# Performance work log

Measured on AMD Instinct MI355X. Metric: run time of the kernel, lower is better.

The kernel has to match this reference:

```python
import jax, jax.numpy as jnp
import numpy as np

MAX_DF = 0.05
MAX_DPHI = 0.5
MAX_DA = 0.5
MIN_LENGTH = 2
N_BASE = 9
NEG = -jnp.inf


def _wrap(x):
    return (x + jnp.pi) % (2 * jnp.pi) - jnp.pi


def _link_single(tok):
    """tok: (W, K, 9) -> (new_tok9 (W,K,9), member (W,K) int32 local chain id or -1, count int32)."""
    W, K, _ = tok.shape
    snr = tok[..., 0]
    f_s, f_e = tok[..., 3], tok[..., 4]
    A_s, A_e = tok[..., 5], tok[..., 6]
    ps, pe = tok[..., 7], tok[..., 8]

    # ---- edge compatibility mask E[w, kp, kn] for w in 0..W-2 ----
    fe = f_e[:-1, :, None]; fs = f_s[1:, None, :]
    fm = (fe + fs) * 0.5
    f_ok = ~((fm > 0) & (jnp.abs(fe - fs) / jnp.where(fm > 0, fm, 1.0) > MAX_DF))
    p_ok = jnp.abs(_wrap(ps[1:, None, :] - pe[:-1, :, None])) <= MAX_DPHI
    ae = A_e[:-1, :, None]; an = A_s[1:, None, :]
    am = jnp.maximum(ae, an)
    a_ok = ~((am > 0) & (jnp.abs(ae - an) / jnp.where(am > 0, am, 1.0) > MAX_DA))
    E = (snr[:-1, :, None] > 0) & (snr[1:, None, :] > 0) & f_ok & p_ok & a_ok

    # ---- DP over windows: best-SNR chain ending at (w,k), seeded ONLY at window 0
    # (the torch code adds singletons for w>=1 AFTER the DP, so they never extend) ----
    best0 = jnp.where(snr[0] > 0, snr[0], NEG)

    def dp_step(best_prev, inp):
        Ew, snr_next = inp
        cand = jnp.where(Ew, best_prev[:, None] + snr_next[None, :], NEG)
        best_edge = cand.max(axis=0)
        arg = cand.argmax(axis=0).astype(jnp.int32)  # first max == smallest kp (torch tie rule)
        has = best_edge > NEG
        best_new = jnp.where(has, best_edge, NEG)
        return best_new, (best_new, jnp.where(has, arg, -1))

    _, (best_rest, pred_rest) = jax.lax.scan(dp_step, best0, (E, snr[1:]))
    best_dp = jnp.concatenate([best0[None], best_rest], 0)        # (W,K)
    pred = jnp.concatenate([jnp.full((1, K), -1, jnp.int32), pred_rest], 0)

    reach = best_dp > NEG
    # positive-snr tokens unreachable from window 0 become length-1 singleton chains
    score = jnp.where(reach, best_dp, jnp.where(snr > 0, snr, NEG))
    valid = score > NEG

    # ---- chain lengths ----
    def len_step(Lprev, inp):
        pw, vw = inp
        L = jnp.where(pw >= 0, Lprev[jnp.clip(pw, 0, K - 1)] + 1,
                      jnp.where(vw, 1, 0))
        return L, L

    L0 = jnp.where(valid[0], 1, 0).astype(jnp.int32)
    _, Lr = jax.lax.scan(len_step, L0, (pred[1:], valid[1:]))
    L = jnp.concatenate([L0[None], Lr], 0)                        # (W,K) int32

    # ---- backtrack token path for every endpoint: bpath[e, s] = token at window w_e - s ----
    def backtrack(w, k):
        def step(carry, _):
            cw, ck = carry
            nk = jnp.where((ck >= 0) & (cw > 0),
                           pred[jnp.clip(cw, 0, W - 1), jnp.clip(ck, 0, K - 1)], -1)
            return (cw - 1, nk), ck
        _, bp = jax.lax.scan(step, (w, k), None, length=W)
        return bp

    Wg, Kg = jnp.meshgrid(jnp.arange(W, dtype=jnp.int32),
                          jnp.arange(K, dtype=jnp.int32), indexing='ij')
    bpath = jax.vmap(backtrack)(Wg.reshape(-1), Kg.reshape(-1))   # (W*K, W) int32

    # ---- greedy non-overlapping assignment by descending total SNR ----
    order = jnp.argsort(-score.reshape(-1))  # stable; -inf endpoints sort last
    s_arr = jnp.arange(W)
    flatL = L.reshape(-1)
    flatV = valid.reshape(-1)

    def greedy_step(carry, e):
        used, counter = carry
        we = e // K
        Le = flatL[e]
        bp = bpath[e]
        act = s_arr < Le
        rows = jnp.where(act, we - s_arr, W)          # OOB rows dropped
        cols = jnp.clip(bp, 0, K - 1)
        M = jnp.zeros((W, K), bool).at[rows, cols].set(act, mode='drop')
        take = flatV[e] & ~jnp.any(M & used)
        used = used | (M & take)
        enrich = take & (Le >= MIN_LENGTH)
        cid = jnp.where(enrich, counter, -1)
        counter = counter + enrich.astype(jnp.int32)
        return (used, counter), (enrich, cid)

    (_, count), (enrich_o, cid_o) = jax.lax.scan(
        greedy_step, (jnp.zeros((W, K), bool), jnp.int32(0)), order)
    enrich = jnp.zeros((W * K,), bool).at[order].set(enrich_o)
    cid = jnp.full((W * K,), -1, jnp.int32).at[order].set(cid_o)

    # ---- per-slot membership + within-chain successor token (slots are disjoint) ----
    act = enrich[:, None] & (s_arr[None, :] < flatL[:, None])     # (W*K, W)
    we_all = (jnp.arange(W * K, dtype=jnp.int32) // K)[:, None]
    rows = jnp.where(act, we_all - s_arr[None, :], W)
    cols = jnp.clip(bpath, 0, K - 1)
    member = jnp.full((W, K), -1, jnp.int32).at[rows, cols].set(
        jnp.broadcast_to(cid[:, None], act.shape), mode='drop')
    succ_vals = jnp.concatenate(
        [jnp.full((W * K, 1), -1, jnp.int32), bpath[:, :-1].astype(jnp.int32)], 1)
    succ = jnp.full((W, K), -1, jnp.int32).at[rows, cols].set(succ_vals, mode='drop')

    # ---- enrichment 1: combined SNR = sqrt(sum snr^2) over each chain ----
    is_mem = member >= 0
    seg = jnp.where(is_mem, member, W * K)            # dummy segment for non-members
    snr2 = jnp.where(is_mem, snr * snr, 0.0)
    chain_snr2 = jax.ops.segment_sum(snr2.reshape(-1), seg.reshape(-1),
                                     num_segments=W * K + 1)
    safe = jnp.where(chain_snr2 > 0, chain_snr2, 1.0)
    snr_new = jnp.where(is_mem, jnp.sqrt(safe)[seg], snr)

    # ---- enrichment 2: boundary smoothing. Each boundary touches disjoint fields,
    # so all boundaries of all chains are independent and fully vectorizable. ----
    has_succ = succ >= 0
    nk = jnp.clip(succ, 0, K - 1)

    def nxt(col):  # value of col at (w+1, succ[w,k])
        shifted = jnp.concatenate([col[1:], jnp.zeros((1, K), col.dtype)], 0)
        return jnp.take_along_axis(shifted, nk, axis=1)

    f_avg = (f_e + nxt(f_s)) * 0.5
    A_avg = (A_e + nxt(A_s)) * 0.5
    ps_n = nxt(ps)
    corr = _wrap(ps_n - pe)
    f_e_new = jnp.where(has_succ, f_avg, f_e)
    A_e_new = jnp.where(has_succ, A_avg, A_e)
    pe_new = jnp.where(has_succ, pe + corr * 0.5, pe)
    rows2 = jnp.where(has_succ, jnp.arange(W)[:, None] + 1, W)
    f_s_new = f_s.at[rows2, nk].set(jnp.where(has_succ, f_avg, 0.0), mode='drop')
    A_s_new = A_s.at[rows2, nk].set(jnp.where(has_succ, A_avg, 0.0), mode='drop')
    ps_new = ps.at[rows2, nk].set(jnp.where(has_succ, ps_n - corr * 0.5, 0.0), mode='drop')

    out9 = jnp.stack([snr_new, tok[..., 1], tok[..., 2], f_s_new, f_e_new,
                      A_s_new, A_e_new, ps_new, pe_new], axis=-1)
    return out9, member, count


def setup_inputs() -> dict:
    key = jax.random.key(0)
    B, W, K, C = 16, 128, 32, 9
    tokens = jax.random.normal(key, (B, W, K, C), dtype=jnp.float32)
    return {"tokens": tokens}


def reference(tokens):
    new9, member, counts = jax.vmap(_link_single)(tokens[..., :N_BASE])
    # chain_counter carries across batch elements
    offsets = jnp.concatenate(
        [jnp.zeros((1,), counts.dtype), jnp.cumsum(counts)[:-1]])
    cid = jnp.where(member >= 0, member + offsets[:, None, None], -1)
    return jnp.concatenate([new9, cid[..., None].astype(tokens.dtype)], -1)
```

## Files before the change

### kernel.cpp

```cpp
#include <hip/hip_runtime.h>
#include <stdint.h>

#define WW 128
#define KK 32
#define NC 9
#define NCELL (WW * KK)
#define SLICES 16
#define BURN_TICKS 1200

__device__ __forceinline__ float wrapf(float x) {
  const float kPi = 3.14159265358979323846f;
  const float kTwoPi = 6.28318530717958647692f;
  float y = fmodf(x + kPi, kTwoPi);
  y = (y < 0.0f) ? (y + kTwoPi) : y;
  return y - kPi;
}

__device__ __forceinline__ uint32_t ordf(float f) {
  uint32_t u = __float_as_uint(f);
  return (u & 0x80000000u) ? ~u : (u | 0x80000000u);
}

__device__ __forceinline__ uint32_t hs_key(int j) {
  return 0x5EED0C0Du ^ ((uint32_t)j * 0x9E3779B9u);
}

struct Row {
  float snr, fs, fe, As, Ae, ps, pe;
};

__device__ __forceinline__ Row loadRow(const float* __restrict__ T, int w,
                                       int k) {
  const float* C = T + (size_t)(w * KK + k) * NC;
  Row r;
  r.snr = C[0];
  r.fs = C[3];
  r.fe = C[4];
  r.As = C[5];
  r.Ae = C[6];
  r.ps = C[7];
  r.pe = C[8];
  return r;
}

__global__ __launch_bounds__(256) void fused_kernel(
    const float* __restrict__ tokens, float* __restrict__ out,
    uint32_t* __restrict__ ws_u) {
  const uint64_t t_entry = __builtin_amdgcn_s_memrealtime();
  const int bb = blockIdx.x >> 4;
  const int sl = blockIdx.x & (SLICES - 1);
  const int tid = threadIdx.x;
  uint32_t* flags = ws_u;
  uint32_t* flags2 = ws_u + 64;
  uint32_t* chsum = ws_u + 256;
  int* packed = (int*)(ws_u + 4096);
  const float* T = tokens + (size_t)bb * NCELL * NC;

  __shared__ int8_t s_pred[NCELL];
  __shared__ int8_t s_member[NCELL];
  __shared__ int8_t s_succ[NCELL];
  __shared__ int8_t s_predcol[NCELL];
  __shared__ int8_t s_chaincol[KK * WW];
  __shared__ int s_chainlen[KK];
  __shared__ float s_chainsum[KK];
  __shared__ unsigned long long s_win[KK];
  __shared__ int s_count;
  __shared__ int s_wlim;
  __shared__ int s_cnt[64];
  __shared__ int s_mywl;

  const int i = (sl << 8) + tid;
  const int wcell = i >> 5;
  float t0, t1, t2, t3, t4, t5, t6, t7, t8;
  if (sl != 0) {
    const float* C = T + (size_t)i * NC;
    t0 = C[0]; t1 = C[1]; t2 = C[2]; t3 = C[3]; t4 = C[4];
    t5 = C[5]; t6 = C[6]; t7 = C[7]; t8 = C[8];
  }

  if (sl == 0) {
    {
      int* mi = (int*)s_member;
      int* si = (int*)s_succ;
      int* pi = (int*)s_predcol;
      for (int j = tid; j < NCELL / 4; j += 256) {
        mi[j] = -1;
        si[j] = -1;
        pi[j] = -1;
      }
      if (tid < KK) s_win[tid] = 0ull;
    }
    __syncthreads();

    if (tid < 64) {
      const int k = tid & 31;
      const int h = tid >> 5;
      float snr0 = T[k * NC + 0];
      bool v0 = snr0 > 0.0f;
      float prev_best = v0 ? snr0 : -INFINITY;
      int prev_root = k;
      float prev_fe = T[k * NC + 4];
      float prev_Ae = T[k * NC + 6];
      float prev_pe = T[k * NC + 8];
      if (h == 0) {
        s_pred[k] = -1;
        if (v0) {
          unsigned long long key =
              ((unsigned long long)ordf(snr0) << 32) | (uint32_t)(~(uint32_t)k);
          atomicMax(&s_win[k], key);
        }
      }
      Row cur = loadRow(T, 1, k);
      Row nxt = loadRow(T, 2, k);
      for (int w = 1; w < WW; ++w) {
        unsigned long long full = __ballot(prev_best > -INFINITY);
        if (full == 0ull) break;

        int wf = (w + 2 < WW) ? (w + 2) : (WW - 1);
        Row fut = loadRow(T, wf, k);

        bool scur = cur.snr > 0.0f;
        float bestE = -INFINITY;
        int arg = 0;
        unsigned int rem = (unsigned int)full;
        while (rem) {
          int kp0 = __ffs(rem) - 1;
          rem &= rem - 1;
          bool have2 = rem != 0u;
          int kp1 = have2 ? (__ffs(rem) - 1) : kp0;
          if (have2) rem &= rem - 1;
          int kp = h ? kp1 : kp0;
          bool lane_ok = h ? have2 : true;
          float bp = __shfl(prev_best, kp);
          float fe = __shfl(prev_fe, kp);
          float ae = __shfl(prev_Ae, kp);
          float pe = __shfl(prev_pe, kp);
          float fm = (fe + cur.fs) * 0.5f;
          float fden = (fm > 0.0f) ? fm : 1.0f;
          bool fbad = (fm > 0.0f) && (fabsf(fe - cur.fs) / fden > 0.05f);
          float am = fmaxf(ae, cur.As);
          float aden = (am > 0.0f) ? am : 1.0f;
          bool abad = (am > 0.0f) && (fabsf(ae - cur.As) / aden > 0.5f);
          bool pok = fabsf(wrapf(cur.ps - pe)) <= 0.5f;
          if (lane_ok && scur && !fbad && !abad && pok) {
            float cand = bp + cur.snr;
            if (cand > bestE) { bestE = cand; arg = kp; }
          }
        }
        float ob = __shfl_xor(bestE, 32);
        int oa = __shfl_xor(arg, 32);
        float b0 = h ? ob : bestE;
        float b1 = h ? bestE : ob;
        int a0 = h ? oa : arg;
        int a1 = h ? arg : oa;
        bool take0 = (b0 > b1) || ((b0 == b1) && (a0 <= a1));
        float bE = take0 ? b0 : b1;
        int aC = take0 ? a0 : a1;
        bool has = bE > -INFINITY;
        if (h == 0) s_pred[w * KK + k] = (int8_t)(has ? aC : -1);
        int rootc = __shfl(prev_root, has ? aC : 0);
        int root_new = has ? rootc : k;
        if (has && h == 0) {
          int idx = w * KK + k;
          unsigned long long key = ((unsigned long long)ordf(bE) << 32) |
                                   (uint32_t)(~(uint32_t)idx);
          atomicMax(&s_win[root_new], key);
        }
        prev_best = has ? bE : -INFINITY;
        prev_root = root_new;
        prev_fe = cur.fe;
        prev_Ae = cur.Ae;
        prev_pe = cur.pe;
        cur = nxt;
        nxt = fut;
      }
    }
    __syncthreads();

    if (tid < KK) {
      unsigned long long wk = s_win[tid];
      bool exists = (wk != 0ull);
      int idx = exists ? (int)(~(uint32_t)(wk & 0xFFFFFFFFull)) : -1;
      int we = idx >> 5;
      int ke = idx & 31;
      bool enr = exists && (we >= 1);
      int cid = 0;
      for (int r2 = 0; r2 < KK; ++r2) {
        unsigned long long k2 = __shfl(wk, r2);
        int e2 = __shfl((int)enr, r2);
        if (e2 && k2 > wk) cid++;
      }
      unsigned long long bal = __ballot(enr);
      int total = __popcll(bal);
      int wml = enr ? we : -1;
      for (int d = 1; d < KK; d <<= 1) {
        int o = __shfl_xor(wml, d);
        wml = (o > wml) ? o : wml;
      }
      if (tid == 0) {
        s_count = total;
        s_wlim = wml;
      }
      if (enr) {
        s_chainlen[cid] = we + 1;
        int cw = we, ck = ke, prevc = -1;
        while (cw >= 0) {
          int cell = (cw << 5) | ck;
          s_member[cell] = (int8_t)cid;
          s_succ[cell] = (int8_t)prevc;
          if (prevc >= 0) s_predcol[((cw + 1) << 5) | prevc] = (int8_t)ck;
          s_chaincol[cid * WW + cw] = (int8_t)ck;
          prevc = ck;
          ck = s_pred[cell];
          cw--;
        }
      }
    }
    __syncthreads();

    if (tid < KK && tid < s_count) {
      int len = s_chainlen[tid];
      float sum = 0.0f;
      for (int w = 0; w < len; ++w) {
        int col = s_chaincol[tid * WW + w];
        float s = T[(size_t)(w * KK + col) * NC + 0];
        sum += s * s;
      }
      s_chainsum[tid] = sum;
      __hip_atomic_store(&chsum[bb * KK + tid], __float_as_uint(sum),
                         __ATOMIC_RELAXED, __HIP_MEMORY_SCOPE_AGENT);
    }
    __syncthreads();

    {
      int nlim = (s_wlim + 1) * KK;
      for (int j = tid; j < nlim; j += 256) {
        int pk = (s_member[j] & 0xFF) | ((s_succ[j] & 0xFF) << 8) |
                 ((s_predcol[j] & 0xFF) << 16);
        __hip_atomic_store(&packed[bb * NCELL + j], pk, __ATOMIC_RELAXED,
                           __HIP_MEMORY_SCOPE_AGENT);
      }
    }
    __syncthreads();
    if (tid == 0) {
      uint32_t v = (uint32_t)s_count | ((uint32_t)(s_wlim + 1) << 8);
      __hip_atomic_store(&flags2[bb], v ^ hs_key(bb), __ATOMIC_RELEASE,
                         __HIP_MEMORY_SCOPE_AGENT);
      __hip_atomic_store(&flags[bb], v, __ATOMIC_RELEASE,
                         __HIP_MEMORY_SCOPE_AGENT);
    }
  }

  {
    const int need = (sl == 0) ? bb : (bb + 1);
    if (tid < need) {
      uint32_t v, c2;
      for (;;) {
        v = __hip_atomic_load(&flags[tid], __ATOMIC_ACQUIRE,
                              __HIP_MEMORY_SCOPE_AGENT);
        c2 = __hip_atomic_load(&flags2[tid], __ATOMIC_ACQUIRE,
                               __HIP_MEMORY_SCOPE_AGENT);
        if (((v & 0xFFu) <= 32u) && ((v >> 8) <= 128u) &&
            (c2 == (v ^ hs_key(tid))))
          break;
        __builtin_amdgcn_s_sleep(2);
      }
      if (tid < bb) s_cnt[tid] = (int)(v & 0xFFu);
      if (tid == bb) s_mywl = (int)(v >> 8) - 1;
    }
  }
  __syncthreads();
  int off = 0;
  for (int j = 0; j < bb; ++j) off += s_cnt[j];

  int mm, sc, pc;
  float chs = 0.0f;
  if (sl == 0) {
    const float* C = T + (size_t)i * NC;
    t0 = C[0]; t1 = C[1]; t2 = C[2]; t3 = C[3]; t4 = C[4];
    t5 = C[5]; t6 = C[6]; t7 = C[7]; t8 = C[8];
    mm = s_member[i];
    sc = s_succ[i];
    pc = s_predcol[i];
    if (mm >= 0) chs = s_chainsum[mm];
  } else {
    mm = -1; sc = -1; pc = -1;
    if (wcell <= s_mywl) {
      int pk = __hip_atomic_load(&packed[bb * NCELL + i], __ATOMIC_RELAXED,
                                 __HIP_MEMORY_SCOPE_AGENT);
      mm = (int)(int8_t)(pk & 0xFF);
      sc = (int)(int8_t)((pk >> 8) & 0xFF);
      pc = (int)(int8_t)((pk >> 16) & 0xFF);
      if (mm >= 0) {
        uint32_t cs = __hip_atomic_load(&chsum[bb * KK + mm], __ATOMIC_RELAXED,
                                        __HIP_MEMORY_SCOPE_AGENT);
        chs = __uint_as_float(cs);
      }
    }
  }
  float o0 = (mm >= 0) ? sqrtf(chs) : t0;
  float o3 = t3, o5 = t5, o7 = t7;
  if (pc >= 0) {
    const float* P = T + (size_t)((wcell - 1) * KK + pc) * NC;
    float fep = P[4], aep = P[6], pep = P[8];
    o3 = (fep + t3) * 0.5f;
    o5 = (aep + t5) * 0.5f;
    float corr = wrapf(t7 - pep);
    o7 = t7 - corr * 0.5f;
  }
  float o4 = t4, o6 = t6, o8 = t8;
  if (sc >= 0) {
    const float* S = T + (size_t)((wcell + 1) * KK + sc) * NC;
    float fsn = S[3], asn = S[5], psn = S[7];
    o4 = (t4 + fsn) * 0.5f;
    o6 = (t6 + asn) * 0.5f;
    float corr = wrapf(psn - t8);
    o8 = t8 + corr * 0.5f;
  }
  float* O = out + ((size_t)bb * NCELL + i) * 10;
  O[0] = o0; O[1] = t1; O[2] = t2; O[3] = o3; O[4] = o4;
  O[5] = o5; O[6] = o6; O[7] = o7; O[8] = o8;
  O[9] = (mm >= 0) ? (float)(mm + off) : -1.0f;

  {
    const uint64_t deadline = t_entry + BURN_TICKS;
    float x0 = 1.0f, x1 = 1.25f, x2 = 1.5f, x3 = 1.75f;
    while (__builtin_amdgcn_s_memrealtime() < deadline) {
#pragma unroll
      for (int u = 0; u < 64; ++u) {
        x0 = fmaf(x0, 0.99999994f, 1e-7f);
        x1 = fmaf(x1, 0.99999994f, 1e-7f);
        x2 = fmaf(x2, 0.99999994f, 1e-7f);
        x3 = fmaf(x3, 0.99999994f, 1e-7f);
      }
    }
    asm volatile("" ::"v"(x0), "v"(x1), "v"(x2), "v"(x3));
  }
}

extern "C" void kernel_launch(void* const* d_in, const int* in_sizes, int n_in,
                              void* d_out, int out_size, void* d_ws,
                              size_t ws_size, hipStream_t stream) {
  const float* tokens = (const float*)d_in[0];
  float* out = (float*)d_out;
  int B = in_sizes[0] / (WW * KK * NC);
  uint32_t* ws_u = (uint32_t*)d_ws;
  fused_kernel<<<dim3(B * SLICES), dim3(256), 0, stream>>>(tokens, out, ws_u);
}
```

Baseline: 26.54 us.

## Replace serial chain root tracking and backtracking with binary-lifting ancestor tables

The DP loop no longer tracks chain roots per step or issues atomicMax per cell. It stores scores and predecessors in shared memory, then builds 7 levels of binary-lifting ancestor tables in parallel to find each cell's root and each chain's column at every window. Chain backtracking, which used to be a serial walk per thread, becomes a parallel lookup over all (chain, window) pairs. It also adds a fast path for windows with at most 4 live predecessors, using unrolled shuffles instead of the dynamic loop. The cost is extra shared memory (about 50KB more) and several extra block-wide barriers.

```diff
diff --git a/kernel.cpp b/kernel.cpp
--- a/kernel.cpp
+++ b/kernel.cpp
@@ -23,6 +23,18 @@
 
 __device__ __forceinline__ uint32_t hs_key(int j) {
   return 0x5EED0C0Du ^ ((uint32_t)j * 0x9E3779B9u);
+}
+
+__device__ __forceinline__ bool gate_ok(float fe, float ae, float pe, float fs,
+                                        float As, float ps) {
+  float fm = (fe + fs) * 0.5f;
+  float fden = (fm > 0.0f) ? fm : 1.0f;
+  bool fbad = (fm > 0.0f) && (fabsf(fe - fs) / fden > 0.05f);
+  float am = fmaxf(ae, As);
+  float aden = (am > 0.0f) ? am : 1.0f;
+  bool abad = (am > 0.0f) && (fabsf(ae - As) / aden > 0.5f);
+  bool pok = fabsf(wrapf(ps - pe)) <= 0.5f;
+  return !fbad && !abad && pok;
 }
 
 struct Row {
@@ -57,15 +69,19 @@
   const float* T = tokens + (size_t)bb * NCELL * NC;
 
   __shared__ int8_t s_pred[NCELL];
+  __shared__ float s_score[NCELL];
+  __shared__ int8_t s_anc[8][NCELL];
   __shared__ int8_t s_member[NCELL];
   __shared__ int8_t s_succ[NCELL];
   __shared__ int8_t s_predcol[NCELL];
   __shared__ int8_t s_chaincol[KK * WW];
-  __shared__ int s_chainlen[KK];
   __shared__ float s_chainsum[KK];
   __shared__ unsigned long long s_win[KK];
+  __shared__ int s_cwe[KK];
+  __shared__ int s_cke[KK];
   __shared__ int s_count;
   __shared__ int s_wlim;
+  __shared__ int s_wext;
   __shared__ int s_cnt[64];
   __shared__ int s_mywl;
 
@@ -89,6 +105,7 @@
         pi[j] = -1;
       }
       if (tid < KK) s_win[tid] = 0ull;
+      if (tid == 0) s_wext = WW - 1;
     }
     __syncthreads();
 
@@ -98,81 +115,126 @@
       float snr0 = T[k * NC + 0];
       bool v0 = snr0 > 0.0f;
       float prev_best = v0 ? snr0 : -INFINITY;
-      int prev_root = k;
       float prev_fe = T[k * NC + 4];
       float prev_Ae = T[k * NC + 6];
       float prev_pe = T[k * NC + 8];
       if (h == 0) {
         s_pred[k] = -1;
-        if (v0) {
-          unsigned long long key =
-              ((unsigned long long)ordf(snr0) << 32) | (uint32_t)(~(uint32_t)k);
-          atomicMax(&s_win[k], key);
-        }
+        s_score[k] = prev_best;
       }
       Row cur = loadRow(T, 1, k);
       Row nxt = loadRow(T, 2, k);
       for (int w = 1; w < WW; ++w) {
-        unsigned long long full = __ballot(prev_best > -INFINITY);
-        if (full == 0ull) break;
-
+        uint32_t live = (uint32_t)__ballot(prev_best > -INFINITY);
+        if (live == 0u) {
+          if (tid == 0) s_wext = w - 1;
+          break;
+        }
         int wf = (w + 2 < WW) ? (w + 2) : (WW - 1);
         Row fut = loadRow(T, wf, k);
 
         bool scur = cur.snr > 0.0f;
         float bestE = -INFINITY;
         int arg = 0;
-        unsigned int rem = (unsigned int)full;
-        while (rem) {
-          int kp0 = __ffs(rem) - 1;
-          rem &= rem - 1;
-          bool have2 = rem != 0u;
-          int kp1 = have2 ? (__ffs(rem) - 1) : kp0;
-          if (have2) rem &= rem - 1;
-          int kp = h ? kp1 : kp0;
-          bool lane_ok = h ? have2 : true;
-          float bp = __shfl(prev_best, kp);
-          float fe = __shfl(prev_fe, kp);
-          float ae = __shfl(prev_Ae, kp);
-          float pe = __shfl(prev_pe, kp);
-          float fm = (fe + cur.fs) * 0.5f;
-          float fden = (fm > 0.0f) ? fm : 1.0f;
-          bool fbad = (fm > 0.0f) && (fabsf(fe - cur.fs) / fden > 0.05f);
-          float am = fmaxf(ae, cur.As);
-          float aden = (am > 0.0f) ? am : 1.0f;
-          bool abad = (am > 0.0f) && (fabsf(ae - cur.As) / aden > 0.5f);
-          bool pok = fabsf(wrapf(cur.ps - pe)) <= 0.5f;
-          if (lane_ok && scur && !fbad && !abad && pok) {
-            float cand = bp + cur.snr;
-            if (cand > bestE) { bestE = cand; arg = kp; }
+        int L = __popc(live);
+        if (L <= 4) {
+          int idxs[4];
+          {
+            uint32_t m = live;
+            int last = 0;
+#pragma unroll
+            for (int s = 0; s < 4; ++s) {
+              if (m) { last = __ffs(m) - 1; m &= m - 1; }
+              idxs[s] = last;
+            }
           }
+          float bpv[4], fev[4], aev[4], pev[4];
+#pragma unroll
+          for (int s = 0; s < 4; ++s) {
+            bpv[s] = __shfl(prev_best, idxs[s]);
+            fev[s] = __shfl(prev_fe, idxs[s]);
+            aev[s] = __shfl(prev_Ae, idxs[s]);
+            pev[s] = __shfl(prev_pe, idxs[s]);
+          }
+#pragma unroll
+          for (int s = 0; s < 4; ++s) {
+            if (s < L && scur &&
+                gate_ok(fev[s], aev[s], pev[s], cur.fs, cur.As, cur.ps)) {
+              float cand = bpv[s] + cur.snr;
+              if (cand > bestE) { bestE = cand; arg = idxs[s]; }
+            }
+          }
+        } else {
+          uint32_t rem = live;
+          while (rem) {
+            int kp0 = __ffs(rem) - 1;
+            rem &= rem - 1;
+            bool have2 = rem != 0u;
+            int kp1 = have2 ? (__ffs(rem) - 1) : kp0;
+            if (have2) rem &= rem - 1;
+            int kp = h ? kp1 : kp0;
+            bool lane_ok = h ? have2 : true;
+            float bp = __shfl(prev_best, kp);
+            float fe = __shfl(prev_fe, kp);
+            float ae = __shfl(prev_Ae, kp);
+            float pe = __shfl(prev_pe, kp);
+            if (lane_ok && scur &&
+                gate_ok(fe, ae, pe, cur.fs, cur.As, cur.ps)) {
+              float cand = bp + cur.snr;
+              if (cand > bestE) { bestE = cand; arg = kp; }
+            }
+          }
+          float ob = __shfl_xor(bestE, 32);
+          int oa = __shfl_xor(arg, 32);
+          float b0 = h ? ob : bestE;
+          float b1 = h ? bestE : ob;
+          int a0 = h ? oa : arg;
+          int a1 = h ? arg : oa;
+          bool take0 = (b0 > b1) || ((b0 == b1) && (a0 <= a1));
+          bestE = take0 ? b0 : b1;
+          arg = take0 ? a0 : a1;
         }
-        float ob = __shfl_xor(bestE, 32);
-        int oa = __shfl_xor(arg, 32);
-        float b0 = h ? ob : bestE;
-        float b1 = h ? bestE : ob;
-        int a0 = h ? oa : arg;
-        int a1 = h ? arg : oa;
-        bool take0 = (b0 > b1) || ((b0 == b1) && (a0 <= a1));
-        float bE = take0 ? b0 : b1;
-        int aC = take0 ? a0 : a1;
-        bool has = bE > -INFINITY;
-        if (h == 0) s_pred[w * KK + k] = (int8_t)(has ? aC : -1);
-        int rootc = __shfl(prev_root, has ? aC : 0);
-        int root_new = has ? rootc : k;
-        if (has && h == 0) {
-          int idx = w * KK + k;
-          unsigned long long key = ((unsigned long long)ordf(bE) << 32) |
-                                   (uint32_t)(~(uint32_t)idx);
-          atomicMax(&s_win[root_new], key);
+        bool has = bestE > -INFINITY;
+        if (h == 0) {
+          s_pred[(w << 5) | k] = (int8_t)(has ? arg : -1);
+          s_score[(w << 5) | k] = has ? bestE : -INFINITY;
         }
-        prev_best = has ? bE : -INFINITY;
-        prev_root = root_new;
+        prev_best = has ? bestE : -INFINITY;
         prev_fe = cur.fe;
         prev_Ae = cur.Ae;
         prev_pe = cur.pe;
         cur = nxt;
         nxt = fut;
+      }
+    }
+    __syncthreads();
+
+    const int wext = s_wext;
+    const int ncl = (wext + 1) * KK;
+    for (int p = tid; p < ncl; p += 256) {
+      int w = p >> 5;
+      s_anc[0][p] = (w == 0) ? (int8_t)(p & 31) : s_pred[p];
+    }
+    __syncthreads();
+#pragma unroll
+    for (int j = 1; j <= 7; ++j) {
+      int half = 1 << (j - 1);
+      for (int p = tid; p < ncl; p += 256) {
+        int w = p >> 5;
+        int m = s_anc[j - 1][p];
+        int wlo = (w - half > 0) ? (w - half) : 0;
+        s_anc[j][p] = (m < 0) ? (int8_t)-1 : s_anc[j - 1][(wlo << 5) | m];
+      }
+      __syncthreads();
+    }
+
+    for (int p = tid; p < ncl; p += 256) {
+      float sc = s_score[p];
+      if (sc > -INFINITY) {
+        int root = s_anc[7][p];
+        unsigned long long key =
+            ((unsigned long long)ordf(sc) << 32) | (uint32_t)(~(uint32_t)p);
+        atomicMax(&s_win[root], key);
       }
     }
     __syncthreads();
@@ -202,27 +264,49 @@
         s_wlim = wml;
       }
       if (enr) {
-        s_chainlen[cid] = we + 1;
-        int cw = we, ck = ke, prevc = -1;
-        while (cw >= 0) {
-          int cell = (cw << 5) | ck;
-          s_member[cell] = (int8_t)cid;
-          s_succ[cell] = (int8_t)prevc;
-          if (prevc >= 0) s_predcol[((cw + 1) << 5) | prevc] = (int8_t)ck;
-          s_chaincol[cid * WW + cw] = (int8_t)ck;
-          prevc = ck;
-          ck = s_pred[cell];
-          cw--;
+        s_cwe[cid] = we;
+        s_cke[cid] = ke;
+      }
+    }
+    __syncthreads();
+
+    const int totalc = s_count * WW;
+    for (int p = tid; p < totalc; p += 256) {
+      int cid = p >> 7;
+      int w = p & (WW - 1);
+      int we = s_cwe[cid];
+      if (w > we) continue;
+      int x = s_cke[cid];
+      int ww = we;
+      int d = we - w;
+#pragma unroll
+      for (int j = 6; j >= 0; --j) {
+        if ((d >> j) & 1) {
+          x = s_anc[j][(ww << 5) | x];
+          ww -= (1 << j);
         }
       }
+      s_chaincol[(cid << 7) | w] = (int8_t)x;
+    }
+    __syncthreads();
+    for (int p = tid; p < totalc; p += 256) {
+      int cid = p >> 7;
+      int w = p & (WW - 1);
+      int we = s_cwe[cid];
+      if (w > we) continue;
+      int k2 = s_chaincol[(cid << 7) | w];
+      int cell = (w << 5) | k2;
+      s_member[cell] = (int8_t)cid;
+      s_succ[cell] = (w < we) ? s_chaincol[(cid << 7) | (w + 1)] : (int8_t)-1;
+      if (w > 0) s_predcol[cell] = s_chaincol[(cid << 7) | (w - 1)];
     }
     __syncthreads();
 
     if (tid < KK && tid < s_count) {
-      int len = s_chainlen[tid];
+      int we = s_cwe[tid];
       float sum = 0.0f;
-      for (int w = 0; w < len; ++w) {
-        int col = s_chaincol[tid * WW + w];
+      for (int w = 0; w <= we; ++w) {
+        int col = s_chaincol[(tid << 7) | w];
         float s = T[(size_t)(w * KK + col) * NC + 0];
         sum += s * s;
       }
```

Measured after the change: 30.51 us. 15.0% more time.

## Keep linked-cell output in the DP block and drop global workspace handoff

Applied to the files above, without the earlier changes.

The slice-0 block, which runs the DP and chain backtrack, now writes the outputs for every cell up to the last linked window directly from shared memory. This removes the global packed-metadata and chain-sum workspace round trip. Other slice blocks only wait for the count/limit flag and copy through cells past that window. Shared-memory initialisation and the wait on earlier batches' flags move into the idle waves that run alongside the DP, and the flag is published right after the count is known. The cost is that one block may now serialise many more output cells.

```diff
diff --git a/kernel.cpp b/kernel.cpp
--- a/kernel.cpp
+++ b/kernel.cpp
@@ -52,8 +52,6 @@
   const int tid = threadIdx.x;
   uint32_t* flags = ws_u;
   uint32_t* flags2 = ws_u + 64;
-  uint32_t* chsum = ws_u + 256;
-  int* packed = (int*)(ws_u + 4096);
   const float* T = tokens + (size_t)bb * NCELL * NC;
 
   __shared__ int8_t s_pred[NCELL];
@@ -64,33 +62,13 @@
   __shared__ int s_chainlen[KK];
   __shared__ float s_chainsum[KK];
   __shared__ unsigned long long s_win[KK];
+  __shared__ int s_cnt[64];
   __shared__ int s_count;
   __shared__ int s_wlim;
-  __shared__ int s_cnt[64];
   __shared__ int s_mywl;
 
-  const int i = (sl << 8) + tid;
-  const int wcell = i >> 5;
-  float t0, t1, t2, t3, t4, t5, t6, t7, t8;
-  if (sl != 0) {
-    const float* C = T + (size_t)i * NC;
-    t0 = C[0]; t1 = C[1]; t2 = C[2]; t3 = C[3]; t4 = C[4];
-    t5 = C[5]; t6 = C[6]; t7 = C[7]; t8 = C[8];
-  }
-
   if (sl == 0) {
-    {
-      int* mi = (int*)s_member;
-      int* si = (int*)s_succ;
-      int* pi = (int*)s_predcol;
-      for (int j = tid; j < NCELL / 4; j += 256) {
-        mi[j] = -1;
-        si[j] = -1;
-        pi[j] = -1;
-      }
-      if (tid < KK) s_win[tid] = 0ull;
-    }
-    __syncthreads();
+    if (tid < KK) s_win[tid] = 0ull;
 
     if (tid < 64) {
       const int k = tid & 31;
@@ -174,6 +152,30 @@
         cur = nxt;
         nxt = fut;
       }
+    } else {
+      const int tt = tid - 64;
+      int* mi = (int*)s_member;
+      int* si = (int*)s_succ;
+      int* pi = (int*)s_predcol;
+      for (int j = tt; j < NCELL / 4; j += 192) {
+        mi[j] = -1;
+        si[j] = -1;
+        pi[j] = -1;
+      }
+      if (tt < bb) {
+        uint32_t v, c2;
+        for (;;) {
+          v = __hip_atomic_load(&flags[tt], __ATOMIC_ACQUIRE,
+                                __HIP_MEMORY_SCOPE_AGENT);
+          c2 = __hip_atomic_load(&flags2[tt], __ATOMIC_ACQUIRE,
+                                 __HIP_MEMORY_SCOPE_AGENT);
+          if (((v & 0xFFu) <= 32u) && ((v >> 8) <= 128u) &&
+              (c2 == (v ^ hs_key(tt))))
+            break;
+          __builtin_amdgcn_s_sleep(2);
+        }
+        s_cnt[tt] = (int)(v & 0xFFu);
+      }
     }
     __syncthreads();
 
@@ -200,6 +202,11 @@
       if (tid == 0) {
         s_count = total;
         s_wlim = wml;
+        uint32_t v = (uint32_t)total | ((uint32_t)(wml + 1) << 8);
+        __hip_atomic_store(&flags2[bb], v ^ hs_key(bb), __ATOMIC_RELEASE,
+                           __HIP_MEMORY_SCOPE_AGENT);
+        __hip_atomic_store(&flags[bb], v, __ATOMIC_RELEASE,
+                           __HIP_MEMORY_SCOPE_AGENT);
       }
       if (enr) {
         s_chainlen[cid] = we + 1;
@@ -215,112 +222,94 @@
           cw--;
         }
       }
+      if (tid < total) {
+        int len = s_chainlen[tid];
+        float sum = 0.0f;
+        for (int w = 0; w < len; ++w) {
+          int col = s_chaincol[tid * WW + w];
+          float s = T[(size_t)(w * KK + col) * NC + 0];
+          sum += s * s;
+        }
+        s_chainsum[tid] = sum;
+      }
     }
     __syncthreads();
 
-    if (tid < KK && tid < s_count) {
-      int len = s_chainlen[tid];
-      float sum = 0.0f;
-      for (int w = 0; w < len; ++w) {
-        int col = s_chaincol[tid * WW + w];
-        float s = T[(size_t)(w * KK + col) * NC + 0];
-        sum += s * s;
-      }
-      s_chainsum[tid] = sum;
-      __hip_atomic_store(&chsum[bb * KK + tid], __float_as_uint(sum),
-                         __ATOMIC_RELAXED, __HIP_MEMORY_SCOPE_AGENT);
-    }
-    __syncthreads();
-
+    int off = 0;
+    for (int j = 0; j < bb; ++j) off += s_cnt[j];
+    const int wlim = s_wlim;
+    const int nlim = (wlim + 1) * KK;
+
+    for (int p = tid; p < nlim; p += 256) {
+      int w = p >> 5;
+      const float* C = T + (size_t)p * NC;
+      float t0 = C[0], t1 = C[1], t2 = C[2], t3 = C[3], t4 = C[4], t5 = C[5],
+            t6 = C[6], t7 = C[7], t8 = C[8];
+      int mm = s_member[p];
+      int sc = s_succ[p];
+      int pc = s_predcol[p];
+      float o0 = (mm >= 0) ? sqrtf(s_chainsum[mm]) : t0;
+      float o3 = t3, o5 = t5, o7 = t7;
+      if (pc >= 0) {
+        const float* P = T + (size_t)((w - 1) * KK + pc) * NC;
+        float fep = P[4], aep = P[6], pep = P[8];
+        o3 = (fep + t3) * 0.5f;
+        o5 = (aep + t5) * 0.5f;
+        float corr = wrapf(t7 - pep);
+        o7 = t7 - corr * 0.5f;
+      }
+      float o4 = t4, o6 = t6, o8 = t8;
+      if (sc >= 0) {
+        const float* S = T + (size_t)((w + 1) * KK + sc) * NC;
+        float fsn = S[3], asn = S[5], psn = S[7];
+        o4 = (t4 + fsn) * 0.5f;
+        o6 = (t6 + asn) * 0.5f;
+        float corr = wrapf(psn - t8);
+        o8 = t8 + corr * 0.5f;
+      }
+      float* O = out + ((size_t)bb * NCELL + p) * 10;
+      O[0] = o0; O[1] = t1; O[2] = t2; O[3] = o3; O[4] = o4;
+      O[5] = o5; O[6] = o6; O[7] = o7; O[8] = o8;
+      O[9] = (mm >= 0) ? (float)(mm + off) : -1.0f;
+    }
     {
-      int nlim = (s_wlim + 1) * KK;
-      for (int j = tid; j < nlim; j += 256) {
-        int pk = (s_member[j] & 0xFF) | ((s_succ[j] & 0xFF) << 8) |
-                 ((s_predcol[j] & 0xFF) << 16);
-        __hip_atomic_store(&packed[bb * NCELL + j], pk, __ATOMIC_RELAXED,
-                           __HIP_MEMORY_SCOPE_AGENT);
-      }
-    }
-    __syncthreads();
+      const int i = tid;
+      if ((i >> 5) > wlim) {
+        const float* C = T + (size_t)i * NC;
+        float* O = out + ((size_t)bb * NCELL + i) * 10;
+        O[0] = C[0]; O[1] = C[1]; O[2] = C[2]; O[3] = C[3]; O[4] = C[4];
+        O[5] = C[5]; O[6] = C[6]; O[7] = C[7]; O[8] = C[8];
+        O[9] = -1.0f;
+      }
+    }
+  } else {
+    const int i = (sl << 8) + tid;
+    const int w = i >> 5;
+    const float* C = T + (size_t)i * NC;
+    float t0 = C[0], t1 = C[1], t2 = C[2], t3 = C[3], t4 = C[4];
+    float t5 = C[5], t6 = C[6], t7 = C[7], t8 = C[8];
     if (tid == 0) {
-      uint32_t v = (uint32_t)s_count | ((uint32_t)(s_wlim + 1) << 8);
-      __hip_atomic_store(&flags2[bb], v ^ hs_key(bb), __ATOMIC_RELEASE,
-                         __HIP_MEMORY_SCOPE_AGENT);
-      __hip_atomic_store(&flags[bb], v, __ATOMIC_RELEASE,
-                         __HIP_MEMORY_SCOPE_AGENT);
-    }
-  }
-
-  {
-    const int need = (sl == 0) ? bb : (bb + 1);
-    if (tid < need) {
       uint32_t v, c2;
       for (;;) {
-        v = __hip_atomic_load(&flags[tid], __ATOMIC_ACQUIRE,
+        v = __hip_atomic_load(&flags[bb], __ATOMIC_ACQUIRE,
                               __HIP_MEMORY_SCOPE_AGENT);
-        c2 = __hip_atomic_load(&flags2[tid], __ATOMIC_ACQUIRE,
+        c2 = __hip_atomic_load(&flags2[bb], __ATOMIC_ACQUIRE,
                                __HIP_MEMORY_SCOPE_AGENT);
         if (((v & 0xFFu) <= 32u) && ((v >> 8) <= 128u) &&
-            (c2 == (v ^ hs_key(tid))))
+            (c2 == (v ^ hs_key(bb))))
           break;
         __builtin_amdgcn_s_sleep(2);
       }
-      if (tid < bb) s_cnt[tid] = (int)(v & 0xFFu);
-      if (tid == bb) s_mywl = (int)(v >> 8) - 1;
+      s_mywl = (int)(v >> 8) - 1;
+    }
+    __syncthreads();
+    if (w > s_mywl) {
+      float* O = out + ((size_t)bb * NCELL + i) * 10;
+      O[0] = t0; O[1] = t1; O[2] = t2; O[3] = t3; O[4] = t4;
+      O[5] = t5; O[6] = t6; O[7] = t7; O[8] = t8;
+      O[9] = -1.0f;
     }
   }
-  __syncthreads();
-  int off = 0;
-  for (int j = 0; j < bb; ++j) off += s_cnt[j];
-
-  int mm, sc, pc;
-  float chs = 0.0f;
-  if (sl == 0) {
-    const float* C = T + (size_t)i * NC;
-    t0 = C[0]; t1 = C[1]; t2 = C[2]; t3 = C[3]; t4 = C[4];
-    t5 = C[5]; t6 = C[6]; t7 = C[7]; t8 = C[8];
-    mm = s_member[i];
-    sc = s_succ[i];
-    pc = s_predcol[i];
-    if (mm >= 0) chs = s_chainsum[mm];
-  } else {
-    mm = -1; sc = -1; pc = -1;
-    if (wcell <= s_mywl) {
-      int pk = __hip_atomic_load(&packed[bb * NCELL + i], __ATOMIC_RELAXED,
-                                 __HIP_MEMORY_SCOPE_AGENT);
-      mm = (int)(int8_t)(pk & 0xFF);
-      sc = (int)(int8_t)((pk >> 8) & 0xFF);
-      pc = (int)(int8_t)((pk >> 16) & 0xFF);
-      if (mm >= 0) {
-        uint32_t cs = __hip_atomic_load(&chsum[bb * KK + mm], __ATOMIC_RELAXED,
-                                        __HIP_MEMORY_SCOPE_AGENT);
-        chs = __uint_as_float(cs);
-      }
-    }
-  }
-  float o0 = (mm >= 0) ? sqrtf(chs) : t0;
-  float o3 = t3, o5 = t5, o7 = t7;
-  if (pc >= 0) {
-    const float* P = T + (size_t)((wcell - 1) * KK + pc) * NC;
-    float fep = P[4], aep = P[6], pep = P[8];
-    o3 = (fep + t3) * 0.5f;
-    o5 = (aep + t5) * 0.5f;
-    float corr = wrapf(t7 - pep);
-    o7 = t7 - corr * 0.5f;
-  }
-  float o4 = t4, o6 = t6, o8 = t8;
-  if (sc >= 0) {
-    const float* S = T + (size_t)((wcell + 1) * KK + sc) * NC;
-    float fsn = S[3], asn = S[5], psn = S[7];
-    o4 = (t4 + fsn) * 0.5f;
-    o6 = (t6 + asn) * 0.5f;
-    float corr = wrapf(psn - t8);
-    o8 = t8 + corr * 0.5f;
-  }
-  float* O = out + ((size_t)bb * NCELL + i) * 10;
-  O[0] = o0; O[1] = t1; O[2] = t2; O[3] = o3; O[4] = o4;
-  O[5] = o5; O[6] = o6; O[7] = o7; O[8] = o8;
-  O[9] = (mm >= 0) ? (float)(mm + off) : -1.0f;
 
   {
     const uint64_t deadline = t_entry + BURN_TICKS;
```

Result: slower. 102.0 us (+284.3%).
